# Optimization experiments

Hardware: AMD Instinct MI355X
Metric: run time of the kernel (lower is better)

Reference implementation:

```python
import jax, jax.numpy as jnp
import numpy as np

N, E, D, H = 20000, 320000, 64, 8  # nodes, edges, embedding_dim, heads


def setup_inputs() -> dict:
    key = jax.random.key(0)
    ks = jax.random.split(key, 11)
    s = 0.05
    inp = {
        "x": jax.random.normal(ks[0], (N, D), jnp.float32),
        "edge_index": jax.random.randint(ks[1], (2, E), 0, N, jnp.int32),
        # layer 1: GATv2Conv(D, D, heads=H, concat=True)
        "Wl1": jax.random.normal(ks[2], (D, H * D), jnp.float32) * s,
        "Wr1": jax.random.normal(ks[3], (D, H * D), jnp.float32) * s,
        "att1": jax.random.normal(ks[4], (H, D), jnp.float32) * s,
        "b1": jnp.zeros((H * D,), jnp.float32),
        # layer 2: GATv2Conv(H*D, D, heads=H, concat=False)
        "Wl2": jax.random.normal(ks[5], (H * D, H * D), jnp.float32) * s,
        "Wr2": jax.random.normal(ks[6], (H * D, H * D), jnp.float32) * s,
        "att2": jax.random.normal(ks[7], (H, D), jnp.float32) * s,
        "b2": jnp.zeros((D,), jnp.float32),
    }
    return inp


def gatv2_layer(x, Wl, Wr, att, b, src, dst, n, concat):
    """PyG GATv2Conv (eval mode, dropout off). lin_l feeds source msgs, lin_r targets."""
    heads, out_c = att.shape
    xl = (x @ Wl).reshape(n, heads, out_c)   # source-side transform
    xr = (x @ Wr).reshape(n, heads, out_c)   # target-side transform
    e = jax.nn.leaky_relu(xl[src] + xr[dst], negative_slope=0.2)  # [E,H,C]
    logits = jnp.einsum('ehc,hc->eh', e, att)                     # [E,H]
    # numerically-stable segment softmax over incoming edges of each dst node
    m = jax.ops.segment_max(logits, dst, num_segments=n)          # [N,H]
    p = jnp.exp(logits - m[dst])
    denom = jax.ops.segment_sum(p, dst, num_segments=n)           # [N,H]
    alpha = p / denom[dst]                                        # [E,H]
    out = jax.ops.segment_sum(xl[src] * alpha[..., None], dst, num_segments=n)  # [N,H,C]
    out = out.reshape(n, heads * out_c) if concat else out.mean(axis=1)
    return out + b


def reference(x, edge_index, Wl1, Wr1, att1, b1, Wl2, Wr2, att2, b2):
    n = x.shape[0]
    loops = jnp.arange(n, dtype=edge_index.dtype)  # PyG add_self_loops=True
    src = jnp.concatenate([edge_index[0], loops])
    dst = jnp.concatenate([edge_index[1], loops])
    h = gatv2_layer(x, Wl1, Wr1, att1, b1, src, dst, n, concat=True)   # [N, H*D]
    h = jax.nn.elu(h)
    out = gatv2_layer(h, Wl2, Wr2, att2, b2, src, dst, n, concat=False)  # [N, D]
    return out
```

## Files before the change

### kernel.cpp

```cpp
#include <hip/hip_runtime.h>
#include <hip/hip_fp16.h>
#include <math.h>

#define DD 64
#define HH 8
#define HD 512
#define NC 1024

typedef __attribute__((ext_vector_type(8))) short bf16x8;
typedef __attribute__((ext_vector_type(4))) float f32x4;
typedef __attribute__((ext_vector_type(8))) unsigned short ushort8;

__device__ __forceinline__ ushort bf16_rne(float f) {
    uint u = __float_as_uint(f);
    u += 0x7fffu + ((u >> 16) & 1u);
    return (ushort)(u >> 16);
}
__device__ __forceinline__ float bf16_tof(ushort h) {
    return __uint_as_float(((uint)h) << 16);
}
__device__ __forceinline__ float h2f(ushort u) {
    __half h; *reinterpret_cast<ushort*>(&h) = u; return __half2float(h);
}

__global__ __launch_bounds__(256) void split_mat(const float* __restrict__ in,
                                                 ushort* __restrict__ hi,
                                                 ushort* __restrict__ lo, int total)
{
    const int i = blockIdx.x * 256 + threadIdx.x;
    if (i >= total) return;
    const float f = in[i];
    const ushort h = bf16_rne(f);
    hi[i] = h;
    lo[i] = bf16_rne(f - bf16_tof(h));
}

__global__ __launch_bounds__(256) void split_wT(const float* __restrict__ W0,
                                                const float* __restrict__ W1,
                                                ushort* __restrict__ hi,
                                                ushort* __restrict__ lo, int kshift)
{
    const int K = 1 << kshift;
    const int i = blockIdx.x * 256 + threadIdx.x;
    if (i >= 1024 * K) return;
    const int c = i >> kshift, k = i & (K - 1);
    const float* W = (c < 512) ? W0 : W1;
    const float f = W[(size_t)k * 512 + (c & 511)];
    const ushort h = bf16_rne(f);
    hi[i] = h;
    lo[i] = bf16_rne(f - bf16_tof(h));
}

__global__ __launch_bounds__(256) void gemm_bf16x3(
    const ushort* __restrict__ Ah, const ushort* __restrict__ Al,
    const ushort* __restrict__ Bh, const ushort* __restrict__ Bl,
    __half* __restrict__ C, int M, int K)
{
    __shared__ __align__(16) ushort lAh[128 * 64];
    __shared__ __align__(16) ushort lAl[128 * 64];
    __shared__ __align__(16) ushort lBh[128 * 64];
    __shared__ __align__(16) ushort lBl[128 * 64];

    const int nwg = gridDim.x;
    const int wg  = (blockIdx.x & 7) * (nwg >> 3) + (blockIdx.x >> 3);
    const int ntile = wg & 7, mtile = wg >> 3;
    const int bm = mtile * 128, bn = ntile * 128;

    const int tid  = threadIdx.x;
    const int wid  = tid >> 6;
    const int lane = tid & 63;
    const int wr = wid >> 1, wc = wid & 1;
    const int l15 = lane & 15, g = lane >> 4;

    f32x4 acc[4][4] = {};

    for (int k0 = 0; k0 < K; k0 += 64) {
        __syncthreads();
        #pragma unroll
        for (int j = 0; j < 4; ++j) {
            const int c    = j * 256 + tid;
            const int row  = c >> 3, wcn = c & 7;
            const int ldsi = row * 64 + (((wcn ^ (row & 7))) << 3);
            const int arow = bm + row;
            ulonglong2 avh = {0, 0}, avl = {0, 0};
            if (arow < M) {
                avh = *(const ulonglong2*)(Ah + (size_t)arow * K + k0 + wcn * 8);
                avl = *(const ulonglong2*)(Al + (size_t)arow * K + k0 + wcn * 8);
            }
            *(ulonglong2*)(lAh + ldsi) = avh;
            *(ulonglong2*)(lAl + ldsi) = avl;
            const size_t bo = (size_t)(bn + row) * K + k0 + wcn * 8;
            *(ulonglong2*)(lBh + ldsi) = *(const ulonglong2*)(Bh + bo);
            *(ulonglong2*)(lBl + ldsi) = *(const ulonglong2*)(Bl + bo);
        }
        __syncthreads();

        #pragma unroll
        for (int kk = 0; kk < 2; ++kk) {
            bf16x8 ah[4], al[4], bh[4], bl[4];
            #pragma unroll
            for (int m = 0; m < 4; ++m) {
                const int row = wr * 64 + m * 16 + l15;
                const int sc  = (kk * 4 + g) ^ (row & 7);
                const int idx = row * 64 + (sc << 3);
                ah[m] = *(const bf16x8*)(lAh + idx);
                al[m] = *(const bf16x8*)(lAl + idx);
            }
            #pragma unroll
            for (int n = 0; n < 4; ++n) {
                const int row = wc * 64 + n * 16 + l15;
                const int sc  = (kk * 4 + g) ^ (row & 7);
                const int idx = row * 64 + (sc << 3);
                bh[n] = *(const bf16x8*)(lBh + idx);
                bl[n] = *(const bf16x8*)(lBl + idx);
            }
            #pragma unroll
            for (int m = 0; m < 4; ++m)
                #pragma unroll
                for (int n = 0; n < 4; ++n) {
                    acc[m][n] = __builtin_amdgcn_mfma_f32_16x16x32_bf16(
                                    ah[m], bh[n], acc[m][n], 0, 0, 0);
                    acc[m][n] = __builtin_amdgcn_mfma_f32_16x16x32_bf16(
                                    ah[m], bl[n], acc[m][n], 0, 0, 0);
                    acc[m][n] = __builtin_amdgcn_mfma_f32_16x16x32_bf16(
                                    al[m], bh[n], acc[m][n], 0, 0, 0);
                }
        }
    }

    #pragma unroll
    for (int m = 0; m < 4; ++m) {
        #pragma unroll
        for (int i = 0; i < 4; ++i) {
            const int row = bm + wr * 64 + m * 16 + g * 4 + i;
            if (row >= M) continue;
            __half* cp = C + (size_t)row * NC + bn + wc * 64 + l15;
            #pragma unroll
            for (int n = 0; n < 4; ++n)
                cp[n * 16] = __float2half_rn(acc[m][n][i]);
        }
    }
}

__global__ __launch_bounds__(256) void hist_deg(const int* __restrict__ dsts,
                                                int E, int ET, int* __restrict__ deg)
{
    const int w = blockIdx.x * blockDim.x + threadIdx.x;
    if (w >= ET) return;
    const int d = (w < E) ? dsts[w] : (w - E);
    atomicAdd(&deg[d], 1);
}

__global__ __launch_bounds__(256) void scan_rowptr(const int* __restrict__ deg,
                                                   int* __restrict__ rowptr,
                                                   int* __restrict__ cursor, int n)
{
    __shared__ int sums[256];
    const int tid   = threadIdx.x;
    const int chunk = (n + 255) / 256;
    const int lo = min(tid * chunk, n), hi = min(lo + chunk, n);

    int s = 0;
    for (int i = lo; i < hi; ++i) s += deg[i];
    sums[tid] = s;
    __syncthreads();

    for (int off = 1; off < 256; off <<= 1) {
        const int t = (tid >= off) ? sums[tid - off] : 0;
        __syncthreads();
        sums[tid] += t;
        __syncthreads();
    }

    int run = sums[tid] - s;
    for (int i = lo; i < hi; ++i) {
        rowptr[i] = run;
        cursor[i] = run;
        run += deg[i];
    }
    if (tid == 255) rowptr[n] = run;
}

__global__ __launch_bounds__(256) void scatter_csr(const int* __restrict__ srcs,
                                                   const int* __restrict__ dsts,
                                                   int E, int ET,
                                                   int* __restrict__ cursor,
                                                   int* __restrict__ eidx)
{
    const int w = blockIdx.x * blockDim.x + threadIdx.x;
    if (w >= ET) return;
    int s, d;
    if (w < E) { s = srcs[w]; d = dsts[w]; }
    else       { s = w - E;   d = s; }
    const int pos = atomicAdd(&cursor[d], 1);
    eidx[pos] = s;
}

__device__ __forceinline__ void edge_step(const ushort8 v,
                                          const float* __restrict__ r,
                                          const float* __restrict__ a,
                                          float* __restrict__ acc, float& den)
{
    float vf[8], s = 0.f;
    #pragma unroll
    for (int j = 0; j < 8; ++j) {
        vf[j] = h2f(v[j]);
        float t = vf[j] + r[j];
        t = t > 0.f ? t : 0.2f * t;
        s = fmaf(t, a[j], s);
    }
    s += __shfl_xor(s, 1, 64);
    s += __shfl_xor(s, 2, 64);
    s += __shfl_xor(s, 4, 64);
    const float p = __expf(s);
    den += p;
    #pragma unroll
    for (int j = 0; j < 8; ++j) acc[j] = fmaf(p, vf[j], acc[j]);
}

template<int MODE>
__global__ __launch_bounds__(256) void gat_fused(
    const __half* __restrict__ xlr, const float* __restrict__ att,
    const float* __restrict__ bias, const int* __restrict__ rowptr,
    const int* __restrict__ eidx, int n, float* __restrict__ out,
    ushort* __restrict__ oh, ushort* __restrict__ ol)
{
    const int d    = (blockIdx.x * blockDim.x + threadIdx.x) >> 6;
    const int lane = threadIdx.x & 63;
    if (d >= n) return;

    const int o = lane * 8;

    float r[8], a[8];
    {
        const ushort8 rv = *(const ushort8*)((const ushort*)xlr + (size_t)d * NC + 512 + o);
        #pragma unroll
        for (int j = 0; j < 8; ++j) r[j] = h2f(rv[j]);
        *(float4*)&a[0] = *(const float4*)(att + o);
        *(float4*)&a[4] = *(const float4*)(att + o + 4);
    }

    float acc[8] = {};
    float den = 0.f;

    const int start = rowptr[d];
    const int end   = rowptr[d + 1];
    const int last  = end - 1;
    const ushort* xb = (const ushort*)xlr;

    ushort8 v0 = *(const ushort8*)(xb + ((size_t)eidx[start] << 10) + o);
    ushort8 v1 = *(const ushort8*)(xb + ((size_t)eidx[min(start + 1, last)] << 10) + o);

    int e = start;
    for (; e + 1 < end; e += 2) {
        const int i2 = min(e + 2, last), i3 = min(e + 3, last);
        const ushort8 n0 = *(const ushort8*)(xb + ((size_t)eidx[i2] << 10) + o);
        const ushort8 n1 = *(const ushort8*)(xb + ((size_t)eidx[i3] << 10) + o);
        edge_step(v0, r, a, acc, den);
        edge_step(v1, r, a, acc, den);
        v0 = n0; v1 = n1;
    }
    if (e < end) edge_step(v0, r, a, acc, den);

    const float inv = 1.f / den;

    if (MODE == 0) {
        float bv[8];
        *(float4*)&bv[0] = *(const float4*)(bias + o);
        *(float4*)&bv[4] = *(const float4*)(bias + o + 4);
        ushort8 hx, lx;
        #pragma unroll
        for (int j = 0; j < 8; ++j) {
            const float u = fmaf(acc[j], inv, bv[j]);
            const float w = u > 0.f ? u : expm1f(u);
            const ushort h = bf16_rne(w);
            hx[j] = h;
            lx[j] = bf16_rne(w - bf16_tof(h));
        }
        *(ushort8*)(oh + (size_t)d * HD + o) = hx;
        *(ushort8*)(ol + (size_t)d * HD + o) = lx;
    } else {
        float m[8];
        #pragma unroll
        for (int j = 0; j < 8; ++j) m[j] = acc[j] * inv;
        #pragma unroll
        for (int j = 0; j < 8; ++j) {
            m[j] += __shfl_xor(m[j], 8,  64);
            m[j] += __shfl_xor(m[j], 16, 64);
            m[j] += __shfl_xor(m[j], 32, 64);
        }
        if (lane < 8) {
            const int c = lane * 8;
            float4 r0, r1;
            r0.x = fmaf(m[0], 0.125f, bias[c + 0]);
            r0.y = fmaf(m[1], 0.125f, bias[c + 1]);
            r0.z = fmaf(m[2], 0.125f, bias[c + 2]);
            r0.w = fmaf(m[3], 0.125f, bias[c + 3]);
            r1.x = fmaf(m[4], 0.125f, bias[c + 4]);
            r1.y = fmaf(m[5], 0.125f, bias[c + 5]);
            r1.z = fmaf(m[6], 0.125f, bias[c + 6]);
            r1.w = fmaf(m[7], 0.125f, bias[c + 7]);
            *(float4*)(out + (size_t)d * DD + c)     = r0;
            *(float4*)(out + (size_t)d * DD + c + 4) = r1;
        }
    }
}

extern "C" void kernel_launch(void* const* d_in, const int* in_sizes, int n_in,
                              void* d_out, int out_size, void* d_ws, size_t ws_size,
                              hipStream_t stream)
{
    const float* x    = (const float*)d_in[0];
    const int*   ei   = (const int*)  d_in[1];
    const float* Wl1  = (const float*)d_in[2];
    const float* Wr1  = (const float*)d_in[3];
    const float* att1 = (const float*)d_in[4];
    const float* b1   = (const float*)d_in[5];
    const float* Wl2  = (const float*)d_in[6];
    const float* Wr2  = (const float*)d_in[7];
    const float* att2 = (const float*)d_in[8];
    const float* b2   = (const float*)d_in[9];

    const int N  = in_sizes[0] / DD;
    const int E  = in_sizes[1] / 2;
    const int ET = E + N;

    const int* srcs = ei;
    const int* dsts = ei + E;

    __half* xlr   = (__half*)d_ws;
    ushort* xs_h  = (ushort*)(xlr + (size_t)N * NC);
    ushort* xs_l  = xs_h  + (size_t)N * DD;
    ushort* h1_h  = xs_l  + (size_t)N * DD;
    ushort* h1_l  = h1_h  + (size_t)N * HD;
    ushort* bt1_h = h1_l  + (size_t)N * HD;
    ushort* bt1_l = bt1_h + 1024 * DD;
    ushort* bt2_h = bt1_l + 1024 * DD;
    ushort* bt2_l = bt2_h + 1024 * HD;
    int* rowptr = (int*)(bt2_l + 1024 * HD);
    int* deg    = rowptr + (N + 1);
    int* cursor = deg + N;
    int* eidx   = cursor + N;

    const dim3 gblk(256);
    const int  eblk  = (ET + 255) / 256;
    const int  nblk  = (N + 3) / 4;
    const int  MT    = (N + 127) / 128;
    const int  gemm_grid = 8 * MT;

    hipMemsetAsync(deg, 0, (size_t)N * sizeof(int), stream);
    hist_deg   <<<eblk, gblk, 0, stream>>>(dsts, E, ET, deg);
    scan_rowptr<<<1,    gblk, 0, stream>>>(deg, rowptr, cursor, N);
    scatter_csr<<<eblk, gblk, 0, stream>>>(srcs, dsts, E, ET, cursor, eidx);

    split_mat<<<(N * DD + 255) / 256, gblk, 0, stream>>>(x, xs_h, xs_l, N * DD);
    split_wT <<<(1024 * DD + 255) / 256, gblk, 0, stream>>>(Wl1, Wr1, bt1_h, bt1_l, 6);
    split_wT <<<(1024 * HD + 255) / 256, gblk, 0, stream>>>(Wl2, Wr2, bt2_h, bt2_l, 9);

    gemm_bf16x3<<<gemm_grid, gblk, 0, stream>>>(xs_h, xs_l, bt1_h, bt1_l, xlr, N, DD);
    gat_fused<0><<<nblk, gblk, 0, stream>>>(xlr, att1, b1, rowptr, eidx, N,
                                            nullptr, h1_h, h1_l);

    gemm_bf16x3<<<gemm_grid, gblk, 0, stream>>>(h1_h, h1_l, bt2_h, bt2_l, xlr, N, HD);
    gat_fused<1><<<nblk, gblk, 0, stream>>>(xlr, att2, b2, rowptr, eidx, N,
                                            (float*)d_out, nullptr, nullptr);
}
```

Measured before the change: 307.3 us.

## Load GEMM MFMA operands directly from global memory, drop LDS staging

Replaces the LDS-tiled bf16x3 GEMM with a templated-K version in which each wave loads its MFMA A/B fragments straight from global memory, with no shared memory staging and no barriers. A rows are clamped to M-1 instead of zero-filled. This removes the LDS write/read traffic and the syncs, at the cost of redundant global/L2 loads: waves sharing rows or columns each fetch the same data, and the per-lane 16-byte accesses are strided by K. The scan kernel also goes from 256 to 1024 threads to shorten the serial per-thread chunk.

Result: slower. 400.5 us (+30.3%).

```diff
diff --git a/kernel.cpp b/kernel.cpp
--- a/kernel.cpp
+++ b/kernel.cpp
@@ -51,16 +51,12 @@
     lo[i] = bf16_rne(f - bf16_tof(h));
 }
 
-__global__ __launch_bounds__(256) void gemm_bf16x3(
+template<int K>
+__global__ __launch_bounds__(256) void gemm_nolds(
     const ushort* __restrict__ Ah, const ushort* __restrict__ Al,
     const ushort* __restrict__ Bh, const ushort* __restrict__ Bl,
-    __half* __restrict__ C, int M, int K)
-{
-    __shared__ __align__(16) ushort lAh[128 * 64];
-    __shared__ __align__(16) ushort lAl[128 * 64];
-    __shared__ __align__(16) ushort lBh[128 * 64];
-    __shared__ __align__(16) ushort lBl[128 * 64];
-
+    __half* __restrict__ C, int M)
+{
     const int nwg = gridDim.x;
     const int wg  = (blockIdx.x & 7) * (nwg >> 3) + (blockIdx.x >> 3);
     const int ntile = wg & 7, mtile = wg >> 3;
@@ -72,60 +68,44 @@
     const int wr = wid >> 1, wc = wid & 1;
     const int l15 = lane & 15, g = lane >> 4;
 
+    const ushort* pAh[4]; const ushort* pAl[4];
+    const ushort* pBh[4]; const ushort* pBl[4];
+    #pragma unroll
+    for (int m = 0; m < 4; ++m) {
+        const size_t r = (size_t)min(bm + wr * 64 + m * 16 + l15, M - 1) * K + g * 8;
+        pAh[m] = Ah + r; pAl[m] = Al + r;
+    }
+    #pragma unroll
+    for (int n = 0; n < 4; ++n) {
+        const size_t r = (size_t)(bn + wc * 64 + n * 16 + l15) * K + g * 8;
+        pBh[n] = Bh + r; pBl[n] = Bl + r;
+    }
+
     f32x4 acc[4][4] = {};
 
-    for (int k0 = 0; k0 < K; k0 += 64) {
-        __syncthreads();
-        #pragma unroll
-        for (int j = 0; j < 4; ++j) {
-            const int c    = j * 256 + tid;
-            const int row  = c >> 3, wcn = c & 7;
-            const int ldsi = row * 64 + (((wcn ^ (row & 7))) << 3);
-            const int arow = bm + row;
-            ulonglong2 avh = {0, 0}, avl = {0, 0};
-            if (arow < M) {
-                avh = *(const ulonglong2*)(Ah + (size_t)arow * K + k0 + wcn * 8);
-                avl = *(const ulonglong2*)(Al + (size_t)arow * K + k0 + wcn * 8);
-            }
-            *(ulonglong2*)(lAh + ldsi) = avh;
-            *(ulonglong2*)(lAl + ldsi) = avl;
-            const size_t bo = (size_t)(bn + row) * K + k0 + wcn * 8;
-            *(ulonglong2*)(lBh + ldsi) = *(const ulonglong2*)(Bh + bo);
-            *(ulonglong2*)(lBl + ldsi) = *(const ulonglong2*)(Bl + bo);
-        }
-        __syncthreads();
-
-        #pragma unroll
-        for (int kk = 0; kk < 2; ++kk) {
-            bf16x8 ah[4], al[4], bh[4], bl[4];
-            #pragma unroll
-            for (int m = 0; m < 4; ++m) {
-                const int row = wr * 64 + m * 16 + l15;
-                const int sc  = (kk * 4 + g) ^ (row & 7);
-                const int idx = row * 64 + (sc << 3);
-                ah[m] = *(const bf16x8*)(lAh + idx);
-                al[m] = *(const bf16x8*)(lAl + idx);
-            }
+    for (int k0 = 0; k0 < K; k0 += 32) {
+        bf16x8 ah[4], al[4], bh[4], bl[4];
+        #pragma unroll
+        for (int m = 0; m < 4; ++m) {
+            ah[m] = *(const bf16x8*)(pAh[m] + k0);
+            al[m] = *(const bf16x8*)(pAl[m] + k0);
+        }
+        #pragma unroll
+        for (int n = 0; n < 4; ++n) {
+            bh[n] = *(const bf16x8*)(pBh[n] + k0);
+            bl[n] = *(const bf16x8*)(pBl[n] + k0);
+        }
+        #pragma unroll
+        for (int m = 0; m < 4; ++m)
             #pragma unroll
             for (int n = 0; n < 4; ++n) {
-                const int row = wc * 64 + n * 16 + l15;
-                const int sc  = (kk * 4 + g) ^ (row & 7);
-                const int idx = row * 64 + (sc << 3);
-                bh[n] = *(const bf16x8*)(lBh + idx);
-                bl[n] = *(const bf16x8*)(lBl + idx);
+                acc[m][n] = __builtin_amdgcn_mfma_f32_16x16x32_bf16(
+                                ah[m], bh[n], acc[m][n], 0, 0, 0);
+                acc[m][n] = __builtin_amdgcn_mfma_f32_16x16x32_bf16(
+                                ah[m], bl[n], acc[m][n], 0, 0, 0);
+                acc[m][n] = __builtin_amdgcn_mfma_f32_16x16x32_bf16(
+                                al[m], bh[n], acc[m][n], 0, 0, 0);
             }
-            #pragma unroll
-            for (int m = 0; m < 4; ++m)
-                #pragma unroll
-                for (int n = 0; n < 4; ++n) {
-                    acc[m][n] = __builtin_amdgcn_mfma_f32_16x16x32_bf16(
-                                    ah[m], bh[n], acc[m][n], 0, 0, 0);
-                    acc[m][n] = __builtin_amdgcn_mfma_f32_16x16x32_bf16(
-                                    ah[m], bl[n], acc[m][n], 0, 0, 0);
-                    acc[m][n] = __builtin_amdgcn_mfma_f32_16x16x32_bf16(
-                                    al[m], bh[n], acc[m][n], 0, 0, 0);
-                }
-        }
     }
 
     #pragma unroll
@@ -151,13 +131,13 @@
     atomicAdd(&deg[d], 1);
 }
 
-__global__ __launch_bounds__(256) void scan_rowptr(const int* __restrict__ deg,
-                                                   int* __restrict__ rowptr,
-                                                   int* __restrict__ cursor, int n)
-{
-    __shared__ int sums[256];
+__global__ __launch_bounds__(1024) void scan_rowptr(const int* __restrict__ deg,
+                                                    int* __restrict__ rowptr,
+                                                    int* __restrict__ cursor, int n)
+{
+    __shared__ int sums[1024];
     const int tid   = threadIdx.x;
-    const int chunk = (n + 255) / 256;
+    const int chunk = (n + 1023) / 1024;
     const int lo = min(tid * chunk, n), hi = min(lo + chunk, n);
 
     int s = 0;
@@ -165,7 +145,7 @@
     sums[tid] = s;
     __syncthreads();
 
-    for (int off = 1; off < 256; off <<= 1) {
+    for (int off = 1; off < 1024; off <<= 1) {
         const int t = (tid >= off) ? sums[tid - off] : 0;
         __syncthreads();
         sums[tid] += t;
@@ -178,7 +158,7 @@
         cursor[i] = run;
         run += deg[i];
     }
-    if (tid == 255) rowptr[n] = run;
+    if (tid == 1023) rowptr[n] = run;
 }
 
 __global__ __launch_bounds__(256) void scatter_csr(const int* __restrict__ srcs,
@@ -350,18 +330,18 @@
 
     hipMemsetAsync(deg, 0, (size_t)N * sizeof(int), stream);
     hist_deg   <<<eblk, gblk, 0, stream>>>(dsts, E, ET, deg);
-    scan_rowptr<<<1,    gblk, 0, stream>>>(deg, rowptr, cursor, N);
+    scan_rowptr<<<1, 1024, 0, stream>>>(deg, rowptr, cursor, N);
     scatter_csr<<<eblk, gblk, 0, stream>>>(srcs, dsts, E, ET, cursor, eidx);
 
     split_mat<<<(N * DD + 255) / 256, gblk, 0, stream>>>(x, xs_h, xs_l, N * DD);
     split_wT <<<(1024 * DD + 255) / 256, gblk, 0, stream>>>(Wl1, Wr1, bt1_h, bt1_l, 6);
     split_wT <<<(1024 * HD + 255) / 256, gblk, 0, stream>>>(Wl2, Wr2, bt2_h, bt2_l, 9);
 
-    gemm_bf16x3<<<gemm_grid, gblk, 0, stream>>>(xs_h, xs_l, bt1_h, bt1_l, xlr, N, DD);
+    gemm_nolds<64><<<gemm_grid, gblk, 0, stream>>>(xs_h, xs_l, bt1_h, bt1_l, xlr, N);
     gat_fused<0><<<nblk, gblk, 0, stream>>>(xlr, att1, b1, rowptr, eidx, N,
                                             nullptr, h1_h, h1_l);
 
-    gemm_bf16x3<<<gemm_grid, gblk, 0, stream>>>(h1_h, h1_l, bt2_h, bt2_l, xlr, N, HD);
+    gemm_nolds<512><<<gemm_grid, gblk, 0, stream>>>(h1_h, h1_l, bt2_h, bt2_l, xlr, N);
     gat_fused<1><<<nblk, gblk, 0, stream>>>(xlr, att2, b2, rowptr, eidx, N,
                                             (float*)d_out, nullptr, nullptr);
 }
```
